# Performance work log

Measured on AMD Instinct MI355X. Metric: run time of the kernel, lower is better.

The kernel has to match this reference:

```python
import jax, jax.numpy as jnp
import numpy as np

N = 50000        # nodes
E = 800000       # edges (before self loops)
IN = 128         # in_channels
HID = 32         # hidden_channels (per head)
HEADS = 4
OUT = 10         # out_channels (classes)
G = 64           # graphs in batch
NEG_SLOPE = 0.2  # PyG GATConv default leaky relu slope


def setup_inputs() -> dict:
    key = jax.random.key(0)
    ks = jax.random.split(key, 12)
    s = 0.05
    return {
        "x": jax.random.normal(ks[0], (N, IN), jnp.float32),
        "W1": jax.random.normal(ks[1], (IN, HEADS * HID), jnp.float32) * s,
        "a1_src": jax.random.normal(ks[2], (HEADS, HID), jnp.float32) * s,
        "a1_dst": jax.random.normal(ks[3], (HEADS, HID), jnp.float32) * s,
        "b1": jnp.zeros((HEADS * HID,), jnp.float32),
        "W2": jax.random.normal(ks[4], (HEADS * HID, HEADS * HID), jnp.float32) * s,
        "a2_src": jax.random.normal(ks[5], (HEADS, HID), jnp.float32) * s,
        "a2_dst": jax.random.normal(ks[6], (HEADS, HID), jnp.float32) * s,
        "b2": jnp.zeros((HEADS * HID,), jnp.float32),
        "Wl": jax.random.normal(ks[7], (HEADS * HID, OUT), jnp.float32) * s,
        "bl": jnp.zeros((OUT,), jnp.float32),
        "edge_index": jax.random.randint(ks[8], (2, E), 0, N, jnp.int32),
        "batch": jnp.sort(jax.random.randint(ks[9], (N,), 0, G, jnp.int32)),
    }


def gat_conv(x, src, dst, W, a_src, a_dst, b):
    """PyG GATConv (concat=True, self loops already in src/dst). Eval mode: no dropout."""
    n = x.shape[0]
    h = (x @ W).reshape(n, HEADS, HID)                       # [N,H,C]
    al_s = jnp.einsum('nhc,hc->nh', h, a_src)                # [N,H]
    al_d = jnp.einsum('nhc,hc->nh', h, a_dst)
    e = jax.nn.leaky_relu(al_s[src] + al_d[dst], NEG_SLOPE)  # [Etot,H]
    # segment softmax over destination node neighborhoods
    m = jax.ops.segment_max(e, dst, num_segments=n)
    m = jnp.where(jnp.isfinite(m), m, 0.0)
    p = jnp.exp(e - m[dst])
    z = jax.ops.segment_sum(p, dst, num_segments=n)
    alpha = p / (z[dst] + 1e-16)                             # [Etot,H]
    out = jax.ops.segment_sum(h[src] * alpha[:, :, None], dst, num_segments=n)
    return out.reshape(n, HEADS * HID) + b


def reference(x, W1, a1_src, a1_dst, b1, W2, a2_src, a2_dst, b2, Wl, bl,
              edge_index, batch):
    n = x.shape[0]
    loops = jnp.arange(n, dtype=edge_index.dtype)
    src = jnp.concatenate([edge_index[0], loops])
    dst = jnp.concatenate([edge_index[1], loops])

    h = jax.nn.elu(gat_conv(x, src, dst, W1, a1_src, a1_dst, b1))
    h = gat_conv(h, src, dst, W2, a2_src, a2_dst, b2)

    # global_mean_pool over graph ids
    counts = jax.ops.segment_sum(jnp.ones((n,), h.dtype), batch, num_segments=G)
    pooled = jax.ops.segment_sum(h, batch, num_segments=G) / jnp.maximum(counts, 1.0)[:, None]

    logits = pooled @ Wl + bl
    return jax.nn.softmax(logits, axis=1)
```

## Files before the change

### kernel.cpp

```cpp
#include <hip/hip_runtime.h>
#include <hip/hip_bf16.h>
#include <math.h>

#define HEADS 4
#define HID 32
#define FDIM 128
#define OUTC 10
#define NEG 0.2f
#define ECAP 512
#define BCAP 5440

typedef __attribute__((ext_vector_type(4))) float f32x4;
typedef __attribute__((ext_vector_type(2))) float f32x2;
typedef __attribute__((ext_vector_type(8))) short bf16x8;

static __device__ __forceinline__ float lrelu(float v) { return v > 0.f ? v : NEG * v; }

static __device__ __forceinline__ unsigned bfr(float f) {
  unsigned u = __float_as_uint(f);
  return (u + 0x7fffu + ((u >> 16) & 1u)) >> 16;
}

#define CHUNK 1024

__global__ __launch_bounds__(256) void k_pre1(
    const int* __restrict__ ei, int* __restrict__ gbcur,
    int* __restrict__ bbuf, int E, int n, int nbin,
    const float* __restrict__ W1, const float* __restrict__ W2,
    const float* __restrict__ a1s, const float* __restrict__ a1d,
    const float* __restrict__ a2s, const float* __restrict__ a2d,
    uint4* __restrict__ WF) {
  __shared__ __align__(16) char sm[4096];
  int bid = blockIdx.x;
  int tid = threadIdx.x;
  if (bid < nbin) {
    int* h = (int*)sm;
    int* cur = (int*)(sm + 1024);
    h[tid] = 0;
    __syncthreads();
    int base = bid * CHUNK;
    int tot = E + n;
    #pragma unroll
    for (int r = 0; r < CHUNK / 256; ++r) {
      int e = base + r * 256 + tid;
      if (e < tot) {
        int dst = (e < E) ? ei[E + e] : (e - E);
        atomicAdd(&h[dst >> 8], 1);
      }
    }
    __syncthreads();
    if (h[tid]) cur[tid] = tid * BCAP + atomicAdd(&gbcur[tid], h[tid]);
    __syncthreads();
    #pragma unroll
    for (int r = 0; r < CHUNK / 256; ++r) {
      int e = base + r * 256 + tid;
      if (e < tot) {
        int src = (e < E) ? ei[e] : (e - E);
        int dst = (e < E) ? ei[E + e] : (e - E);
        int pos = atomicAdd(&cur[dst >> 8], 1);
        bbuf[pos] = src | ((dst & 255) << 16);
      }
    }
  } else {
    float (*wa)[8] = (float(*)[8])sm;
    int pb = bid - nbin;
    int layer = pb / 9;
    int xb = pb - layer * 9;
    const float* W = layer ? W2 : W1;
    #pragma unroll
    for (int q = 0; q < 4; ++q) {
      int e = tid * 4 + q;
      int k = e >> 3, c = e & 7;
      int hh = c & 3;
      const float* av = (c < 4 ? (layer ? a2s : a1s) : (layer ? a2d : a1d)) + hh * 32;
      const float* wr = W + (size_t)k * 128 + hh * 32;
      float s = 0.f;
      #pragma unroll
      for (int j = 0; j < 32; j += 4) {
        float4 wv = *reinterpret_cast<const float4*>(wr + j);
        float4 a4 = *reinterpret_cast<const float4*>(av + j);
        s += wv.x * a4.x + wv.y * a4.y + wv.z * a4.z + wv.w * a4.w;
      }
      wa[k][c] = s;
    }
    __syncthreads();
    int gid = xb * 256 + tid;
    if (gid >= 2304) return;
    int lane = gid & 63, frag = gid >> 6;
    int t = frag / 9, ct = frag - t * 9;
    int quad = lane >> 4, r = lane & 15;
    int kbase = t * 32 + quad * 8;
    unsigned v[8];
    if (ct < 8) {
      int col = ct * 16 + r;
      #pragma unroll
      for (int j = 0; j < 8; ++j) v[j] = bfr(W[(size_t)(kbase + j) * 128 + col]);
    } else if (r < 8) {
      #pragma unroll
      for (int j = 0; j < 8; ++j) v[j] = bfr(wa[kbase + j][r]);
    } else {
      #pragma unroll
      for (int j = 0; j < 8; ++j) v[j] = 0;
    }
    uint4 pk;
    pk.x = v[0] | (v[1] << 16);
    pk.y = v[2] | (v[3] << 16);
    pk.z = v[4] | (v[5] << 16);
    pk.w = v[6] | (v[7] << 16);
    WF[layer * 2304 + gid] = pk;
  }
}

template<bool BF16IN>
static __device__ __forceinline__ void mm_body(
    char* sm, int bid, int tid,
    const void* __restrict__ Xv, const uint4* __restrict__ WF,
    unsigned char* __restrict__ H, float* __restrict__ AL, int n) {
  uint4* wf = (uint4*)sm;
  #pragma unroll
  for (int i = 0; i < 9; ++i) wf[i * 256 + tid] = WF[i * 256 + tid];
  __syncthreads();
  int lane = tid & 63, wid = tid >> 6;
  int quad = lane >> 4, r = lane & 15;
  int rowbase = bid * 64 + wid * 16;
  int arow = rowbase + r;
  int arowc = arow < n ? arow : 0;
  const bf16x8* wfs = (const bf16x8*)wf;

  f32x4 acc[9];
  #pragma unroll
  for (int ct = 0; ct < 9; ++ct) acc[ct] = 0;

  #pragma unroll
  for (int t = 0; t < 4; ++t) {
    bf16x8 a;
    if (BF16IN) {
      const uint4* xp = reinterpret_cast<const uint4*>(Xv) + (size_t)arowc * 16;
      uint4 u = xp[t * 4 + quad];
      a = *reinterpret_cast<const bf16x8*>(&u);
    } else {
      const float* xp = reinterpret_cast<const float*>(Xv) + (size_t)arowc * 128 + quad * 8;
      float4 x0 = *reinterpret_cast<const float4*>(xp + t * 32);
      float4 x1 = *reinterpret_cast<const float4*>(xp + t * 32 + 4);
      a[0] = (short)bfr(x0.x); a[1] = (short)bfr(x0.y);
      a[2] = (short)bfr(x0.z); a[3] = (short)bfr(x0.w);
      a[4] = (short)bfr(x1.x); a[5] = (short)bfr(x1.y);
      a[6] = (short)bfr(x1.z); a[7] = (short)bfr(x1.w);
    }
    #pragma unroll
    for (int ct = 0; ct < 9; ++ct)
      acc[ct] = __builtin_amdgcn_mfma_f32_16x16x32_bf16(
          a, wfs[(t * 9 + ct) * 64 + lane], acc[ct], 0, 0, 0);
  }

  int orow0 = rowbase + quad * 4;
  #pragma unroll
  for (int rr = 0; rr < 4; ++rr) {
    int orow = orow0 + rr;
    if (orow < n) {
      unsigned char* hp = H + (size_t)orow * 128 + r;
      #pragma unroll
      for (int ct = 0; ct < 8; ++ct) {
        unsigned p8 = __builtin_amdgcn_cvt_pk_fp8_f32(acc[ct][rr], acc[ct][rr], 0, false);
        hp[ct * 16] = (unsigned char)(p8 & 0xffu);
      }
      if (r < 8) AL[(size_t)orow * 8 + r] = acc[8][rr];
    }
  }
}

__global__ __launch_bounds__(256) void k_pre2(
    const void* __restrict__ Xv, const uint4* __restrict__ WF,
    unsigned char* __restrict__ H, float* __restrict__ AL, int n, int nmm,
    const int* __restrict__ bbuf, const int* __restrict__ gbcur,
    int* __restrict__ offs, int* __restrict__ csr) {
  __shared__ __align__(16) char sm[36864];
  int bid = blockIdx.x;
  int tid = threadIdx.x;
  if (bid < nmm) {
    mm_body<false>(sm, bid, tid, Xv, WF, H, AL, n);
  } else {
    int b = bid - nmm;
    int* deg = (int*)sm;
    int* sc = deg + 256;
    int* cur = sc + 256;
    int ebeg = b * BCAP;
    int eend = ebeg + gbcur[b];
    deg[tid] = 0;
    __syncthreads();
    for (int i = ebeg + tid; i < eend; i += 256)
      atomicAdd(&deg[bbuf[i] >> 16], 1);
    __syncthreads();
    int v = deg[tid];
    sc[tid] = v;
    __syncthreads();
    #pragma unroll
    for (int off = 1; off < 256; off <<= 1) {
      int t = (tid >= off) ? sc[tid - off] : 0;
      __syncthreads();
      sc[tid] += t;
      __syncthreads();
    }
    int excl = sc[tid] - v;
    int dst0 = b * 256 + tid;
    if (dst0 < n) offs[dst0] = ebeg + excl;
    cur[tid] = ebeg + excl;
    __syncthreads();
    for (int i = ebeg + tid; i < eend; i += 256) {
      int pk = bbuf[i];
      int pos = atomicAdd(&cur[pk >> 16], 1);
      csr[pos] = pk;
    }
  }
}

__global__ __launch_bounds__(256) void k_mm2(
    const void* __restrict__ Xv, const uint4* __restrict__ WF,
    unsigned char* __restrict__ H, float* __restrict__ AL, int n) {
  __shared__ __align__(16) char sm[36864];
  mm_body<true>(sm, blockIdx.x, threadIdx.x, Xv, WF, H, AL, n);
}

template<bool ELU_OUT, bool POOL>
__global__ __launch_bounds__(256) void k_agg(
    const unsigned char* __restrict__ H, const float* __restrict__ AL,
    const int* __restrict__ offs, const int* __restrict__ csr,
    const int* __restrict__ gbcur,
    const float* __restrict__ bias, unsigned short* __restrict__ OUT,
    const int* __restrict__ batch, float* __restrict__ pooled,
    int* __restrict__ gcnt, int n) {
  __shared__ __align__(16) char smem[ECAP * 4 + ECAP * 16];
  int* s_l = (int*)smem;
  float (*p_l)[4] = (float(*)[4])(smem + ECAP * 4);
  float (*o_l)[132] = (float(*)[132])smem;
  __shared__ int g_l[16];
  int tid = threadIdx.x;
  int lane = tid & 63;
  int r = lane & 15;
  int gg = (tid >> 6) * 4 + (lane >> 4);
  int nbase = blockIdx.x * 16;
  int node = nbase + gg;
  bool nvalid = node < n;
  int nodec = nvalid ? node : 0;
  int bkt = nbase >> 8;
  int bend = bkt * BCAP + gbcur[bkt];
  int beg = offs[nodec];
  int nxt = nodec + 1;
  int end = nvalid ? ((nxt >= n || (nxt & 255) == 0) ? bend : offs[nxt]) : beg;
  int ebeg = offs[nbase];
  int nend = nbase + 16;
  int eend = (nend >= n || (nend & 255) == 0) ? bend : offs[nend];
  int hsel = r >> 2;
  const uint2* hb = reinterpret_cast<const uint2*>(H) + r;
  int dbase = bkt * 256;

  if (POOL && r == 0) g_l[gg] = nvalid ? batch[node] : -1;

  float z = 0.f;
  float acc[8];
  #pragma unroll
  for (int k = 0; k < 8; ++k) acc[k] = 0.f;

  for (int c0 = ebeg; c0 < eend; c0 += ECAP) {
    int clen = min(ECAP, eend - c0);
    __syncthreads();
    for (int i = tid; i < clen; i += 256) {
      int v = csr[c0 + i];
      int s = v & 0xffff;
      int d = dbase + (v >> 16);
      float4 as_ = *reinterpret_cast<const float4*>(AL + (size_t)s * 8);
      float4 ad = *reinterpret_cast<const float4*>(AL + (size_t)d * 8 + 4);
      s_l[i] = s;
      float4 p;
      p.x = __expf(lrelu(as_.x + ad.x));
      p.y = __expf(lrelu(as_.y + ad.y));
      p.z = __expf(lrelu(as_.z + ad.z));
      p.w = __expf(lrelu(as_.w + ad.w));
      *reinterpret_cast<float4*>(&p_l[i][0]) = p;
    }
    __syncthreads();
    int lo = max(beg, c0), hi = min(end, c0 + clen);
    int cnt = hi - lo;
    int lbase = lo - c0;
    for (int j0 = 0; j0 < cnt; j0 += 8) {
      int sv[8]; float pv[8]; uint2 uv[8];
      #pragma unroll
      for (int q = 0; q < 8; ++q) {
        int j = j0 + q;
        bool vq = j < cnt;
        int jj = lbase + (vq ? j : j0);
        sv[q] = s_l[jj];
        pv[q] = vq ? p_l[jj][hsel] : 0.f;
      }
      #pragma unroll
      for (int q = 0; q < 8; ++q) uv[q] = hb[(size_t)sv[q] * 16];
      #pragma unroll
      for (int q = 0; q < 8; ++q) {
        float p = pv[q];
        z += p;
        f32x2 h0 = __builtin_amdgcn_cvt_pk_f32_fp8(uv[q].x, false);
        f32x2 h1 = __builtin_amdgcn_cvt_pk_f32_fp8(uv[q].x, true);
        f32x2 h2 = __builtin_amdgcn_cvt_pk_f32_fp8(uv[q].y, false);
        f32x2 h3 = __builtin_amdgcn_cvt_pk_f32_fp8(uv[q].y, true);
        acc[0] = fmaf(p, h0.x, acc[0]); acc[1] = fmaf(p, h0.y, acc[1]);
        acc[2] = fmaf(p, h1.x, acc[2]); acc[3] = fmaf(p, h1.y, acc[3]);
        acc[4] = fmaf(p, h2.x, acc[4]); acc[5] = fmaf(p, h2.y, acc[5]);
        acc[6] = fmaf(p, h3.x, acc[6]); acc[7] = fmaf(p, h3.y, acc[7]);
      }
    }
  }

  float inv = 1.f / (z + 1e-16f);
  int f0 = r * 8;
  float4 b0 = *reinterpret_cast<const float4*>(bias + f0);
  float4 b1 = *reinterpret_cast<const float4*>(bias + f0 + 4);
  float o[8];
  o[0] = acc[0] * inv + b0.x; o[1] = acc[1] * inv + b0.y;
  o[2] = acc[2] * inv + b0.z; o[3] = acc[3] * inv + b0.w;
  o[4] = acc[4] * inv + b1.x; o[5] = acc[5] * inv + b1.y;
  o[6] = acc[6] * inv + b1.z; o[7] = acc[7] * inv + b1.w;
  if (ELU_OUT) {
    #pragma unroll
    for (int k = 0; k < 8; ++k) o[k] = o[k] > 0.f ? o[k] : expm1f(o[k]);
  }

  if (!POOL) {
    if (nvalid) {
      uint4 pk;
      pk.x = bfr(o[0]) | (bfr(o[1]) << 16);
      pk.y = bfr(o[2]) | (bfr(o[3]) << 16);
      pk.z = bfr(o[4]) | (bfr(o[5]) << 16);
      pk.w = bfr(o[6]) | (bfr(o[7]) << 16);
      reinterpret_cast<uint4*>(OUT)[(size_t)node * 16 + r] = pk;
    }
  } else {
    __syncthreads();
    *reinterpret_cast<float4*>(&o_l[gg][f0]) = make_float4(o[0], o[1], o[2], o[3]);
    *reinterpret_cast<float4*>(&o_l[gg][f0 + 4]) = make_float4(o[4], o[5], o[6], o[7]);
    __syncthreads();
    if (tid < 128) {
      int f = tid;
      float accp = 0.f; int cur = -1;
      #pragma unroll
      for (int i = 0; i < 16; ++i) {
        int g = g_l[i];
        if (g != cur) {
          if (cur >= 0) atomicAdd(&pooled[(size_t)cur * 128 + f], accp);
          cur = g; accp = 0.f;
        }
        if (g >= 0) accp += o_l[i][f];
      }
      if (cur >= 0) atomicAdd(&pooled[(size_t)cur * 128 + f], accp);
    } else if (tid == 128) {
      int cur = -1, c = 0;
      #pragma unroll
      for (int i = 0; i < 16; ++i) {
        int g = g_l[i];
        if (g != cur) { if (cur >= 0) atomicAdd(&gcnt[cur], c); cur = g; c = 0; }
        if (g >= 0) ++c;
      }
      if (cur >= 0) atomicAdd(&gcnt[cur], c);
    }
  }
}

__global__ void k_head(const float* __restrict__ pooled, const int* __restrict__ gcnt,
                       const float* __restrict__ Wl, const float* __restrict__ bl,
                       float* __restrict__ out) {
  int g = blockIdx.x;
  int lane = threadIdx.x;
  float cnt = fmaxf((float)gcnt[g], 1.f);
  float pA = pooled[(size_t)g * 128 + lane] / cnt;
  float pB = pooled[(size_t)g * 128 + lane + 64] / cnt;
  float l[OUTC];
  #pragma unroll
  for (int o = 0; o < OUTC; ++o) {
    float s = pA * Wl[lane * OUTC + o] + pB * Wl[(lane + 64) * OUTC + o];
    #pragma unroll
    for (int off = 32; off; off >>= 1) s += __shfl_xor(s, off);
    l[o] = s + bl[o];
  }
  float mx = l[0];
  #pragma unroll
  for (int o = 1; o < OUTC; ++o) mx = fmaxf(mx, l[o]);
  float se = 0.f;
  #pragma unroll
  for (int o = 0; o < OUTC; ++o) { l[o] = __expf(l[o] - mx); se += l[o]; }
  if (lane == 0) {
    float inv = 1.f / se;
    #pragma unroll
    for (int o = 0; o < OUTC; ++o) out[g * OUTC + o] = l[o] * inv;
  }
}

extern "C" void kernel_launch(void* const* d_in, const int* in_sizes, int n_in,
                              void* d_out, int out_size, void* d_ws, size_t ws_size,
                              hipStream_t stream) {
  const float* x   = (const float*)d_in[0];
  const float* W1  = (const float*)d_in[1];
  const float* a1s = (const float*)d_in[2];
  const float* a1d = (const float*)d_in[3];
  const float* b1  = (const float*)d_in[4];
  const float* W2  = (const float*)d_in[5];
  const float* a2s = (const float*)d_in[6];
  const float* a2d = (const float*)d_in[7];
  const float* b2  = (const float*)d_in[8];
  const float* Wl  = (const float*)d_in[9];
  const float* bl  = (const float*)d_in[10];
  const int* ei    = (const int*)d_in[11];
  const int* batch = (const int*)d_in[12];
  const int N = in_sizes[12];
  const int E = in_sizes[11] / 2;
  const int G = out_size / OUTC;
  float* out = (float*)d_out;
  (void)n_in; (void)ws_size;

  const int tot = E + N;
  const int NB = (N + 255) / 256;

  char* w = (char*)d_ws;
  auto alloc = [&](size_t bytes) { char* p = w; w += (bytes + 255) & ~(size_t)255; return (void*)p; };
  unsigned char* H = (unsigned char*)alloc((size_t)N * FDIM);
  unsigned short* ACT = (unsigned short*)alloc((size_t)N * FDIM * sizeof(unsigned short));
  float* AL     = (float*)alloc((size_t)N * 8 * sizeof(float));
  uint4* WF     = (uint4*)alloc(2 * 2304 * sizeof(uint4));
  int*   offs   = (int*)alloc((size_t)N * sizeof(int));
  int*   csr    = (int*)alloc((size_t)NB * BCAP * sizeof(int));
  int*   bbuf   = (int*)alloc((size_t)NB * BCAP * sizeof(int));
  char* z0 = w;
  int*   gbcur  = (int*)alloc(256 * sizeof(int));
  int*   gcnt   = (int*)alloc((size_t)G * sizeof(int));
  float* pooled = (float*)alloc((size_t)G * FDIM * sizeof(float));
  size_t zbytes = (size_t)(w - z0);
  hipMemsetAsync(z0, 0, zbytes, stream);

  int nbin = (tot + CHUNK - 1) / CHUNK;
  int gb = (N + 63) / 64;
  int ab = (N + 15) / 16;

  k_pre1<<<nbin + 18, 256, 0, stream>>>(ei, gbcur, bbuf, E, N, nbin,
                                        W1, W2, a1s, a1d, a2s, a2d, WF);
  k_pre2<<<gb + NB, 256, 0, stream>>>(x, WF, H, AL, N, gb, bbuf, gbcur, offs, csr);

  k_agg<true, false><<<ab, 256, 0, stream>>>(H, AL, offs, csr, gbcur, b1, ACT, batch, pooled, gcnt, N);
  k_mm2<<<gb, 256, 0, stream>>>(ACT, WF + 2304, H, AL, N);
  k_agg<false, true><<<ab, 256, 0, stream>>>(H, AL, offs, csr, gbcur, b2, nullptr, batch, pooled, gcnt, N);

  k_head<<<G, 64, 0, stream>>>(pooled, gcnt, Wl, bl, out);
}
```

Baseline: 203.2 us.

## Fuse layer-2 projection GEMM into layer-1 aggregation epilogue

```diff
diff --git a/kernel.cpp b/kernel.cpp
--- a/kernel.cpp
+++ b/kernel.cpp
@@ -111,10 +111,9 @@
   }
 }
 
-template<bool BF16IN>
 static __device__ __forceinline__ void mm_body(
     char* sm, int bid, int tid,
-    const void* __restrict__ Xv, const uint4* __restrict__ WF,
+    const float* __restrict__ X, const uint4* __restrict__ WF,
     unsigned char* __restrict__ H, float* __restrict__ AL, int n) {
   uint4* wf = (uint4*)sm;
   #pragma unroll
@@ -134,19 +133,13 @@
   #pragma unroll
   for (int t = 0; t < 4; ++t) {
     bf16x8 a;
-    if (BF16IN) {
-      const uint4* xp = reinterpret_cast<const uint4*>(Xv) + (size_t)arowc * 16;
-      uint4 u = xp[t * 4 + quad];
-      a = *reinterpret_cast<const bf16x8*>(&u);
-    } else {
-      const float* xp = reinterpret_cast<const float*>(Xv) + (size_t)arowc * 128 + quad * 8;
-      float4 x0 = *reinterpret_cast<const float4*>(xp + t * 32);
-      float4 x1 = *reinterpret_cast<const float4*>(xp + t * 32 + 4);
-      a[0] = (short)bfr(x0.x); a[1] = (short)bfr(x0.y);
-      a[2] = (short)bfr(x0.z); a[3] = (short)bfr(x0.w);
-      a[4] = (short)bfr(x1.x); a[5] = (short)bfr(x1.y);
-      a[6] = (short)bfr(x1.z); a[7] = (short)bfr(x1.w);
-    }
+    const float* xp = X + (size_t)arowc * 128 + quad * 8;
+    float4 x0 = *reinterpret_cast<const float4*>(xp + t * 32);
+    float4 x1 = *reinterpret_cast<const float4*>(xp + t * 32 + 4);
+    a[0] = (short)bfr(x0.x); a[1] = (short)bfr(x0.y);
+    a[2] = (short)bfr(x0.z); a[3] = (short)bfr(x0.w);
+    a[4] = (short)bfr(x1.x); a[5] = (short)bfr(x1.y);
+    a[6] = (short)bfr(x1.z); a[7] = (short)bfr(x1.w);
     #pragma unroll
     for (int ct = 0; ct < 9; ++ct)
       acc[ct] = __builtin_amdgcn_mfma_f32_16x16x32_bf16(
@@ -170,7 +163,7 @@
 }
 
 __global__ __launch_bounds__(256) void k_pre2(
-    const void* __restrict__ Xv, const uint4* __restrict__ WF,
+    const float* __restrict__ X, const uint4* __restrict__ WF,
     unsigned char* __restrict__ H, float* __restrict__ AL, int n, int nmm,
     const int* __restrict__ bbuf, const int* __restrict__ gbcur,
     int* __restrict__ offs, int* __restrict__ csr) {
@@ -178,7 +171,7 @@
   int bid = blockIdx.x;
   int tid = threadIdx.x;
   if (bid < nmm) {
-    mm_body<false>(sm, bid, tid, Xv, WF, H, AL, n);
+    mm_body(sm, bid, tid, X, WF, H, AL, n);
   } else {
     int b = bid - nmm;
     int* deg = (int*)sm;
@@ -214,19 +207,13 @@
   }
 }
 
-__global__ __launch_bounds__(256) void k_mm2(
-    const void* __restrict__ Xv, const uint4* __restrict__ WF,
-    unsigned char* __restrict__ H, float* __restrict__ AL, int n) {
-  __shared__ __align__(16) char sm[36864];
-  mm_body<true>(sm, blockIdx.x, threadIdx.x, Xv, WF, H, AL, n);
-}
-
-template<bool ELU_OUT, bool POOL>
+template<bool POOL>
 __global__ __launch_bounds__(256) void k_agg(
     const unsigned char* __restrict__ H, const float* __restrict__ AL,
     const int* __restrict__ offs, const int* __restrict__ csr,
-    const int* __restrict__ gbcur,
-    const float* __restrict__ bias, unsigned short* __restrict__ OUT,
+    const int* __restrict__ gbcur, const float* __restrict__ bias,
+    const uint4* __restrict__ WF2, unsigned char* __restrict__ H2,
+    float* __restrict__ AL2,
     const int* __restrict__ batch, float* __restrict__ pooled,
     int* __restrict__ gcnt, int n) {
   __shared__ __align__(16) char smem[ECAP * 4 + ECAP * 16];
@@ -319,19 +306,39 @@
   o[2] = acc[2] * inv + b0.z; o[3] = acc[3] * inv + b0.w;
   o[4] = acc[4] * inv + b1.x; o[5] = acc[5] * inv + b1.y;
   o[6] = acc[6] * inv + b1.z; o[7] = acc[7] * inv + b1.w;
-  if (ELU_OUT) {
+  if (!POOL) {
     #pragma unroll
     for (int k = 0; k < 8; ++k) o[k] = o[k] > 0.f ? o[k] : expm1f(o[k]);
-  }
-
-  if (!POOL) {
-    if (nvalid) {
-      uint4 pk;
-      pk.x = bfr(o[0]) | (bfr(o[1]) << 16);
-      pk.y = bfr(o[2]) | (bfr(o[3]) << 16);
-      pk.z = bfr(o[4]) | (bfr(o[5]) << 16);
-      pk.w = bfr(o[6]) | (bfr(o[7]) << 16);
-      reinterpret_cast<uint4*>(OUT)[(size_t)node * 16 + r] = pk;
+    __syncthreads();
+    *reinterpret_cast<float4*>(&o_l[gg][f0]) = make_float4(o[0], o[1], o[2], o[3]);
+    *reinterpret_cast<float4*>(&o_l[gg][f0 + 4]) = make_float4(o[4], o[5], o[6], o[7]);
+    __syncthreads();
+    int wid = tid >> 6;
+    int quad = lane >> 4;
+    for (int ct = wid; ct < 9; ct += 4) {
+      f32x4 acc2 = 0;
+      #pragma unroll
+      for (int t = 0; t < 4; ++t) {
+        const float* ap = &o_l[r][quad * 8 + t * 32];
+        bf16x8 a;
+        #pragma unroll
+        for (int j = 0; j < 8; ++j) a[j] = (short)bfr(ap[j]);
+        bf16x8 b = *reinterpret_cast<const bf16x8*>(&WF2[(t * 9 + ct) * 64 + lane]);
+        acc2 = __builtin_amdgcn_mfma_f32_16x16x32_bf16(a, b, acc2, 0, 0, 0);
+      }
+      int orow0 = nbase + quad * 4;
+      #pragma unroll
+      for (int rr = 0; rr < 4; ++rr) {
+        int orow = orow0 + rr;
+        if (orow < n) {
+          if (ct < 8) {
+            unsigned p8 = __builtin_amdgcn_cvt_pk_fp8_f32(acc2[rr], acc2[rr], 0, false);
+            H2[(size_t)orow * 128 + ct * 16 + r] = (unsigned char)(p8 & 0xffu);
+          } else if (r < 8) {
+            AL2[(size_t)orow * 8 + r] = acc2[rr];
+          }
+        }
+      }
     }
   } else {
     __syncthreads();
@@ -420,9 +427,10 @@
 
   char* w = (char*)d_ws;
   auto alloc = [&](size_t bytes) { char* p = w; w += (bytes + 255) & ~(size_t)255; return (void*)p; };
-  unsigned char* H = (unsigned char*)alloc((size_t)N * FDIM);
-  unsigned short* ACT = (unsigned short*)alloc((size_t)N * FDIM * sizeof(unsigned short));
+  unsigned char* H  = (unsigned char*)alloc((size_t)N * FDIM);
+  unsigned char* H2 = (unsigned char*)alloc((size_t)N * FDIM);
   float* AL     = (float*)alloc((size_t)N * 8 * sizeof(float));
+  float* AL2    = (float*)alloc((size_t)N * 8 * sizeof(float));
   uint4* WF     = (uint4*)alloc(2 * 2304 * sizeof(uint4));
   int*   offs   = (int*)alloc((size_t)N * sizeof(int));
   int*   csr    = (int*)alloc((size_t)NB * BCAP * sizeof(int));
@@ -442,9 +450,12 @@
                                         W1, W2, a1s, a1d, a2s, a2d, WF);
   k_pre2<<<gb + NB, 256, 0, stream>>>(x, WF, H, AL, N, gb, bbuf, gbcur, offs, csr);
 
-  k_agg<true, false><<<ab, 256, 0, stream>>>(H, AL, offs, csr, gbcur, b1, ACT, batch, pooled, gcnt, N);
-  k_mm2<<<gb, 256, 0, stream>>>(ACT, WF + 2304, H, AL, N);
-  k_agg<false, true><<<ab, 256, 0, stream>>>(H, AL, offs, csr, gbcur, b2, nullptr, batch, pooled, gcnt, N);
+  k_agg<false><<<ab, 256, 0, stream>>>(H, AL, offs, csr, gbcur, b1,
+                                       WF + 2304, H2, AL2,
+                                       batch, nullptr, nullptr, N);
+  k_agg<true><<<ab, 256, 0, stream>>>(H2, AL2, offs, csr, gbcur, b2,
+                                      nullptr, nullptr, nullptr,
+                                      batch, pooled, gcnt, N);
 
   k_head<<<G, 64, 0, stream>>>(pooled, gcnt, Wl, bl, out);
 }
```

Measured after the change: 198.3 us (median of 2 runs). -2.4%, faster.
